# Kernel optimization log

Measured on AMD Instinct MI355X. Metric: run time of the kernel, lower is better.

Reference implementation:

```python
import jax, jax.numpy as jnp
import numpy as np

B = 512
NODES_PER_GRAPH = 256
N = B * NODES_PER_GRAPH
IN_DIM = 128
HID = 128
PAD_VALUE = -10000.0


def setup_inputs() -> dict:
    key = jax.random.key(0)
    ks = jax.random.split(key, 10)
    inp = {
        "last_node_batch": jax.random.normal(ks[0], (B, IN_DIM), jnp.float32),
        "h": jax.random.normal(ks[1], (N, HID), jnp.float32),
        # NodeEmbed: Linear(in_dim, hidden_dim)
        "W_embed": jax.random.normal(ks[2], (IN_DIM, HID), jnp.float32) / np.sqrt(IN_DIM),
        "b_embed": jnp.zeros((HID,), jnp.float32),
        # Linear_3(2H, 2H, 2)
        "W1": jax.random.normal(ks[3], (2 * HID, 2 * HID), jnp.float32) / np.sqrt(2 * HID),
        "b1": jnp.zeros((2 * HID,), jnp.float32),
        "W2": jax.random.normal(ks[4], (2 * HID, 2 * HID), jnp.float32) / np.sqrt(2 * HID),
        "b2": jnp.zeros((2 * HID,), jnp.float32),
        "W3": jax.random.normal(ks[5], (2 * HID, 2), jnp.float32) / np.sqrt(2 * HID),
        "b3": jnp.zeros((2,), jnp.float32),
        # ragged batch encoded as sorted segment ids (graph id per node)
        "segment_ids": jnp.repeat(jnp.arange(B, dtype=jnp.int64), NODES_PER_GRAPH),
        "max_nodes": NODES_PER_GRAPH,
    }
    return inp


def reference(last_node_batch, h, W_embed, b_embed, W1, b1, W2, b2, W3, b3,
              segment_ids, max_nodes):
    n = h.shape[0]
    b = last_node_batch.shape[0]
    # per-graph node embed, broadcast to each node of its graph (repeat+cat loop)
    node_embed = last_node_batch @ W_embed + b_embed          # [B, H]
    bcast = node_embed[segment_ids]                           # [N, H]
    stack = jnp.concatenate([h, bcast], axis=1)               # [N, 2H]
    # Linear_3 MLP
    out = jnp.tanh(stack @ W1 + b1)
    out = jnp.tanh(out @ W2 + b2)
    edges = out @ W3 + b3                                     # [N, 2]
    # unbatch + pad_sequence(padding_value=-10000), then flatten(1, -1)
    counts = jax.ops.segment_sum(jnp.ones((n,), jnp.int32), segment_ids, num_segments=b)
    offsets = jnp.cumsum(counts) - counts                     # start index of each graph
    pos = jnp.arange(n) - offsets[segment_ids]                # position within graph
    padded = jnp.full((b, max_nodes, 2), PAD_VALUE, dtype=edges.dtype)
    padded = padded.at[segment_ids, pos].set(edges)
    return padded.reshape(b, max_nodes * 2)
```

## Files before the change

kernel.cpp:

```cpp
#include <hip/hip_runtime.h>


typedef __attribute__((ext_vector_type(8))) short s16x8;
typedef __attribute__((ext_vector_type(4))) float f32x4;

#define MT   64
#define K2   256
#define HID  128
#define LDK  264

__device__ __forceinline__ float b2f(unsigned short u) {
  return __builtin_bit_cast(float, (unsigned int)u << 16);
}
__device__ __forceinline__ unsigned short f2b(float f) {
  unsigned int u = __builtin_bit_cast(unsigned int, f);
  u += 0x7fffu + ((u >> 16) & 1u);
  return (unsigned short)(u >> 16);
}
__device__ __forceinline__ float fast_tanh(float x) {
  float ax = __builtin_fabsf(x);
  float t  = __builtin_amdgcn_exp2f(ax * -2.885390081777927f);
  float r  = (1.0f - t) * __builtin_amdgcn_rcpf(1.0f + t);
  return __builtin_copysignf(r, x);
}

__global__ void probe_kernel(const unsigned int* __restrict__ wraw,
                             unsigned int* __restrict__ flag) {
  const int t = threadIdx.x;
  unsigned int w = wraw[t];
  unsigned int e = (w >> 7) & 0xFFu;
  unsigned long long m = __ballot(e >= 96 && e < 128);
  if (t == 0) flag[0] = (__popcll(m) >= 32) ? 1u : 0u;
}

__global__ __launch_bounds__(256) void prep_kernel(
    const void* __restrict__ last, const void* __restrict__ Wemb,
    const void* __restrict__ bemb,
    const void* __restrict__ W1, const void* __restrict__ W2,
    const void* __restrict__ b1, const void* __restrict__ b2,
    const void* __restrict__ W3, const void* __restrict__ b3,
    unsigned short* __restrict__ W1T, unsigned short* __restrict__ W2T,
    unsigned short* __restrict__ emb,
    float* __restrict__ bias1f, float* __restrict__ bias2f,
    float* __restrict__ w3fp, float* __restrict__ bias3f,
    const unsigned int* __restrict__ flag)
{
  const int blk = blockIdx.x, t = threadIdx.x;
  const bool is16 = flag[0] != 0u;
  if (blk < 128) {
    const void*     S = (blk < 64) ? W1 : W2;
    unsigned short* D = (blk < 64) ? W1T : W2T;
    const int b  = blk & 63;
    const int k0 = (b & 7) * 32, n0 = (b >> 3) * 32;
    #pragma unroll
    for (int q = 0; q < 4; ++q) {
      int idx = t + 256 * q;
      int ln = idx >> 5, lk = idx & 31;
      unsigned short v;
      if (is16) v = ((const unsigned short*)S)[(k0 + lk) * K2 + (n0 + ln)];
      else      v = f2b(((const float*)S)[(k0 + lk) * K2 + (n0 + ln)]);
      D[(n0 + ln) * K2 + (k0 + lk)] = v;
    }
  } else if (blk < 384) {
    __shared__ float lrow[2][HID];
    const int eb = blk - 128;
    const int half = t >> 7, j = t & 127;
    const int brow = eb * 2 + half;
    lrow[half][j] = is16 ? b2f(((const unsigned short*)last)[brow * HID + j])
                         : ((const float*)last)[brow * HID + j];
    __syncthreads();
    float acc = is16 ? b2f(((const unsigned short*)bemb)[j])
                     : ((const float*)bemb)[j];
    if (is16) {
      const unsigned short* w = (const unsigned short*)Wemb;
      #pragma unroll 4
      for (int k = 0; k < HID; ++k) acc += lrow[half][k] * b2f(w[k * HID + j]);
    } else {
      const float* w = (const float*)Wemb;
      #pragma unroll 4
      for (int k = 0; k < HID; ++k) acc += lrow[half][k] * w[k * HID + j];
    }
    emb[brow * HID + j] = f2b(acc);
  } else {
    if (is16) {
      bias1f[t] = b2f(((const unsigned short*)b1)[t]);
      bias2f[t] = b2f(((const unsigned short*)b2)[t]);
      w3fp[t]       = b2f(((const unsigned short*)W3)[t]);
      w3fp[t + 256] = b2f(((const unsigned short*)W3)[t + 256]);
      if (t < 2) bias3f[t] = b2f(((const unsigned short*)b3)[t]);
    } else {
      bias1f[t] = ((const float*)b1)[t];
      bias2f[t] = ((const float*)b2)[t];
      w3fp[t]       = ((const float*)W3)[t];
      w3fp[t + 256] = ((const float*)W3)[t + 256];
      if (t < 2) bias3f[t] = ((const float*)b3)[t];
    }
  }
}

template <int MODE>
__global__ __launch_bounds__(256, 2) void mlp_kernel(
    const void* __restrict__ h,
    const void* __restrict__ last, const void* __restrict__ Wemb,
    const void* __restrict__ bemb,
    const void* __restrict__ W1raw, const void* __restrict__ b1,
    const void* __restrict__ W2raw, const void* __restrict__ b2,
    const void* __restrict__ W3,   const void* __restrict__ b3,
    const unsigned short* __restrict__ W1T,
    const unsigned short* __restrict__ W2T,
    const unsigned short* __restrict__ embws,
    const float* __restrict__ bias1f, const float* __restrict__ bias2f,
    const float* __restrict__ w3fp,   const float* __restrict__ bias3f,
    void* __restrict__ out,
    const unsigned int* __restrict__ flag)
{
  __shared__ __align__(16) unsigned short smA[MT * LDK];
  __shared__ __align__(16) unsigned short embRow[HID];
  __shared__ float w3s[2 * K2];
  __shared__ float b3s[2];
  __shared__ unsigned int flagLds;

  const int t    = threadIdx.x;
  const int lane = t & 63, wave = t >> 6;
  const int quad = lane >> 4, l16 = lane & 15;
  const int base = blockIdx.x * MT;
  const int seg  = base >> 8;

  bool is16;
  if (MODE == 2) {
    if (t < 64) {
      unsigned int w = ((const unsigned int*)Wemb)[t];
      unsigned int e = (w >> 7) & 0xFFu;
      unsigned long long m = __ballot(e >= 96 && e < 128);
      if (t == 0) flagLds = (__popcll(m) >= 32) ? 1u : 0u;
    }
    __syncthreads();
    is16 = flagLds != 0u;
  } else {
    is16 = flag[0] != 0u;
  }

  if (is16) {
    const uint4* hp = (const uint4*)h;
    #pragma unroll
    for (int i = 0; i < 4; ++i) {
      int id = t + 256 * i;
      int r = id >> 4, c = id & 15;
      *(uint4*)&smA[r * LDK + c * 8] = hp[(size_t)(base + r) * 16 + c];
    }
  } else {
    const float4* hf = (const float4*)h;
    #pragma unroll
    for (int i = 0; i < 8; ++i) {
      int id = t + 256 * i;
      int r = id >> 5, c = id & 31;
      float4 v = hf[(size_t)(base + r) * 32 + c];
      ushort4 u;
      u.x = f2b(v.x); u.y = f2b(v.y); u.z = f2b(v.z); u.w = f2b(v.w);
      *(ushort4*)&smA[r * LDK + c * 4] = u;
    }
  }

  if (MODE == 0) {
    const uint4* ep = (const uint4*)(embws + seg * HID);
    #pragma unroll
    for (int i = 0; i < 4; ++i) {
      int id = t + 256 * i;
      int r = id >> 4, c = id & 15;
      *(uint4*)&smA[r * LDK + HID + c * 8] = ep[c];
    }
  } else {
    if (t < HID) {
      float acc;
      if (is16) {
        acc = b2f(((const unsigned short*)bemb)[t]);
        const unsigned short* lp = (const unsigned short*)last + seg * HID;
        const unsigned short* wp = (const unsigned short*)Wemb;
        #pragma unroll 4
        for (int k = 0; k < HID; ++k) acc += b2f(lp[k]) * b2f(wp[k * HID + t]);
      } else {
        acc = ((const float*)bemb)[t];
        const float* lp = (const float*)last + seg * HID;
        const float* wp = (const float*)Wemb;
        #pragma unroll 4
        for (int k = 0; k < HID; ++k) acc += lp[k] * wp[k * HID + t];
      }
      embRow[t] = f2b(acc);
    }
    __syncthreads();
    #pragma unroll
    for (int i = 0; i < 4; ++i) {
      int id = t + 256 * i;
      int r = id >> 4, c = id & 15;
      *(uint4*)&smA[r * LDK + HID + c * 8] = *(const uint4*)&embRow[c * 8];
    }
  }

  if (MODE == 0) {
    w3s[t] = w3fp[t]; w3s[t + 256] = w3fp[t + 256];
    if (t < 2) b3s[t] = bias3f[t];
  } else {
    if (is16) {
      w3s[t]       = b2f(((const unsigned short*)W3)[t]);
      w3s[t + 256] = b2f(((const unsigned short*)W3)[t + 256]);
      if (t < 2) b3s[t] = b2f(((const unsigned short*)b3)[t]);
    } else {
      w3s[t]       = ((const float*)W3)[t];
      w3s[t + 256] = ((const float*)W3)[t + 256];
      if (t < 2) b3s[t] = ((const float*)b3)[t];
    }
  }
  __syncthreads();

  auto run_layer = [&](const unsigned short* __restrict__ WT,
                       const void* __restrict__ Wraw,
                       const float* __restrict__ biasF,
                       const void* __restrict__ biasRaw) {
    f32x4 acc[4][4];
    #pragma unroll
    for (int i = 0; i < 4; ++i)
      #pragma unroll
      for (int c = 0; c < 4; ++c)
        acc[i][c] = f32x4{0.f, 0.f, 0.f, 0.f};

    #pragma unroll 2
    for (int kk = 0; kk < 8; ++kk) {
      s16x8 a[4], b[4];
      #pragma unroll
      for (int i = 0; i < 4; ++i)
        a[i] = *(const s16x8*)&smA[(i * 16 + l16) * LDK + kk * 32 + quad * 8];
      if (MODE < 2) {
        #pragma unroll
        for (int c = 0; c < 4; ++c)
          b[c] = *(const s16x8*)&WT[(size_t)(wave * 64 + c * 16 + l16) * K2
                                    + kk * 32 + quad * 8];
      } else {
        if (is16) {
          const unsigned short* wp = (const unsigned short*)Wraw;
          #pragma unroll
          for (int c = 0; c < 4; ++c) {
            s16x8 bb;
            #pragma unroll
            for (int j = 0; j < 8; ++j)
              bb[j] = (short)wp[(size_t)(kk * 32 + quad * 8 + j) * K2
                                + wave * 64 + c * 16 + l16];
            b[c] = bb;
          }
        } else {
          const float* wp = (const float*)Wraw;
          #pragma unroll
          for (int c = 0; c < 4; ++c) {
            s16x8 bb;
            #pragma unroll
            for (int j = 0; j < 8; ++j)
              bb[j] = (short)f2b(wp[(size_t)(kk * 32 + quad * 8 + j) * K2
                                    + wave * 64 + c * 16 + l16]);
            b[c] = bb;
          }
        }
      }
      #pragma unroll
      for (int i = 0; i < 4; ++i)
        #pragma unroll
        for (int c = 0; c < 4; ++c)
          acc[i][c] = __builtin_amdgcn_mfma_f32_16x16x32_bf16(
              a[i], b[c], acc[i][c], 0, 0, 0);
    }
    float bl[4];
    #pragma unroll
    for (int c = 0; c < 4; ++c) {
      int n = wave * 64 + c * 16 + l16;
      if (MODE == 0) bl[c] = biasF[n];
      else bl[c] = is16 ? b2f(((const unsigned short*)biasRaw)[n])
                        : ((const float*)biasRaw)[n];
    }
    __syncthreads();
    #pragma unroll
    for (int i = 0; i < 4; ++i)
      #pragma unroll
      for (int c = 0; c < 4; ++c)
        #pragma unroll
        for (int rg = 0; rg < 4; ++rg)
          smA[(i * 16 + quad * 4 + rg) * LDK + wave * 64 + c * 16 + l16] =
              f2b(fast_tanh(acc[i][c][rg] + bl[c]));
    __syncthreads();
  };

  run_layer(W1T, W1raw, bias1f, b1);
  run_layer(W2T, W2raw, bias2f, b2);

  if (t < 128) {
    const int r = t >> 1, e = t & 1;
    float s = b3s[e];
    #pragma unroll 8
    for (int c = 0; c < 32; ++c) {
      s16x8 v = *(const s16x8*)&smA[r * LDK + c * 8];
      #pragma unroll
      for (int i = 0; i < 8; ++i)
        s += b2f((unsigned short)v[i]) * w3s[(c * 8 + i) * 2 + e];
    }
    size_t idx = (size_t)(base + r) * 2 + e;
    if (is16) ((unsigned short*)out)[idx] = f2b(s);
    else      ((float*)out)[idx] = s;
  }
}

extern "C" void kernel_launch(void* const* d_in, const int* in_sizes, int n_in,
                              void* d_out, int out_size, void* d_ws, size_t ws_size,
                              hipStream_t stream) {
  (void)in_sizes; (void)n_in; (void)out_size;
  const void* last = d_in[0];
  const void* h    = d_in[1];
  const void* Wemb = d_in[2];
  const void* bemb = d_in[3];
  const void* W1   = d_in[4];
  const void* b1   = d_in[5];
  const void* W2   = d_in[6];
  const void* b2   = d_in[7];
  const void* W3   = d_in[8];
  const void* b3   = d_in[9];

  char* ws = (char*)d_ws;

  if (ws_size >= 397324) {
    unsigned short* W1T  = (unsigned short*)(ws);
    unsigned short* W2T  = (unsigned short*)(ws + 131072);
    unsigned short* emb  = (unsigned short*)(ws + 262144);
    float* bias1f        = (float*)(ws + 393216);
    float* bias2f        = (float*)(ws + 394240);
    float* w3fp          = (float*)(ws + 395264);
    float* bias3f        = (float*)(ws + 397312);
    unsigned int* flag   = (unsigned int*)(ws + 397320);
    probe_kernel<<<dim3(1), dim3(64), 0, stream>>>((const unsigned int*)Wemb, flag);
    prep_kernel<<<dim3(385), dim3(256), 0, stream>>>(
        last, Wemb, bemb, W1, W2, b1, b2, W3, b3,
        W1T, W2T, emb, bias1f, bias2f, w3fp, bias3f, flag);
    mlp_kernel<0><<<dim3(2048), dim3(256), 0, stream>>>(
        h, last, Wemb, bemb, W1, b1, W2, b2, W3, b3,
        W1T, W2T, emb, bias1f, bias2f, w3fp, bias3f, d_out, flag);
  } else if (ws_size >= 262208) {
    unsigned short* W1T  = (unsigned short*)(ws);
    unsigned short* W2T  = (unsigned short*)(ws + 131072);
    unsigned int* flag   = (unsigned int*)(ws + 262144);
    probe_kernel<<<dim3(1), dim3(64), 0, stream>>>((const unsigned int*)Wemb, flag);
    prep_kernel<<<dim3(128), dim3(256), 0, stream>>>(
        last, Wemb, bemb, W1, W2, b1, b2, W3, b3,
        W1T, W2T, W1T, (float*)ws, (float*)ws, (float*)ws, (float*)ws, flag);
    mlp_kernel<1><<<dim3(2048), dim3(256), 0, stream>>>(
        h, last, Wemb, bemb, W1, b1, W2, b2, W3, b3,
        W1T, W2T, nullptr, nullptr, nullptr, nullptr, nullptr, d_out, flag);
  } else {
    mlp_kernel<2><<<dim3(2048), dim3(256), 0, stream>>>(
        h, last, Wemb, bemb, W1, b1, W2, b2, W3, b3,
        nullptr, nullptr, nullptr, nullptr, nullptr, nullptr, nullptr,
        d_out, nullptr);
  }
}
```

Baseline: 193.9 us.

## Fold graph embedding into per-graph layer-1 bias and fuse into single MLP kernel

The embed half of layer 1 is no longer a GEMM over every node. Each block computes emb @ W1[128:] plus b1 as a per-graph bias, which halves the K of the first MFMA GEMM. The probe and prep kernels are merged into a single packing kernel that writes weights in an MFMA-fragment layout. The main kernel now handles 128-row tiles with 512 threads and splits the output head across four threads per row. Each block recomputes the small per-graph embedding and bias GEMVs, which adds scalar work and a larger LDS footprint per block.

Result: faster. 184.5 us (-4.9%).

```diff
diff --git a/kernel.cpp b/kernel.cpp
--- a/kernel.cpp
+++ b/kernel.cpp
@@ -4,9 +4,8 @@
 typedef __attribute__((ext_vector_type(8))) short s16x8;
 typedef __attribute__((ext_vector_type(4))) float f32x4;
 
-#define MT   64
 #define K2   256
-#define HID  128
+#define KH   128
 #define LDK  264
 
 __device__ __forceinline__ float b2f(unsigned short u) {
@@ -23,128 +22,77 @@
   float r  = (1.0f - t) * __builtin_amdgcn_rcpf(1.0f + t);
   return __builtin_copysignf(r, x);
 }
-
-__global__ void probe_kernel(const unsigned int* __restrict__ wraw,
-                             unsigned int* __restrict__ flag) {
-  const int t = threadIdx.x;
+__device__ __forceinline__ unsigned int probe_is16(const unsigned int* wraw,
+                                                   int t) {
   unsigned int w = wraw[t];
   unsigned int e = (w >> 7) & 0xFFu;
   unsigned long long m = __ballot(e >= 96 && e < 128);
-  if (t == 0) flag[0] = (__popcll(m) >= 32) ? 1u : 0u;
-}
-
-__global__ __launch_bounds__(256) void prep_kernel(
-    const void* __restrict__ last, const void* __restrict__ Wemb,
-    const void* __restrict__ bemb,
+  return (__popcll(m) >= 32) ? 1u : 0u;
+}
+
+__global__ __launch_bounds__(256) void prep_pack(
     const void* __restrict__ W1, const void* __restrict__ W2,
-    const void* __restrict__ b1, const void* __restrict__ b2,
-    const void* __restrict__ W3, const void* __restrict__ b3,
-    unsigned short* __restrict__ W1T, unsigned short* __restrict__ W2T,
-    unsigned short* __restrict__ emb,
-    float* __restrict__ bias1f, float* __restrict__ bias2f,
-    float* __restrict__ w3fp, float* __restrict__ bias3f,
-    const unsigned int* __restrict__ flag)
+    const void* __restrict__ Wemb,
+    unsigned short* __restrict__ W1P, unsigned short* __restrict__ W2P)
 {
+  __shared__ unsigned int flagLds;
   const int blk = blockIdx.x, t = threadIdx.x;
-  const bool is16 = flag[0] != 0u;
-  if (blk < 128) {
-    const void*     S = (blk < 64) ? W1 : W2;
-    unsigned short* D = (blk < 64) ? W1T : W2T;
-    const int b  = blk & 63;
-    const int k0 = (b & 7) * 32, n0 = (b >> 3) * 32;
-    #pragma unroll
-    for (int q = 0; q < 4; ++q) {
-      int idx = t + 256 * q;
-      int ln = idx >> 5, lk = idx & 31;
-      unsigned short v;
-      if (is16) v = ((const unsigned short*)S)[(k0 + lk) * K2 + (n0 + ln)];
-      else      v = f2b(((const float*)S)[(k0 + lk) * K2 + (n0 + ln)]);
-      D[(n0 + ln) * K2 + (k0 + lk)] = v;
-    }
-  } else if (blk < 384) {
-    __shared__ float lrow[2][HID];
-    const int eb = blk - 128;
-    const int half = t >> 7, j = t & 127;
-    const int brow = eb * 2 + half;
-    lrow[half][j] = is16 ? b2f(((const unsigned short*)last)[brow * HID + j])
-                         : ((const float*)last)[brow * HID + j];
-    __syncthreads();
-    float acc = is16 ? b2f(((const unsigned short*)bemb)[j])
-                     : ((const float*)bemb)[j];
-    if (is16) {
-      const unsigned short* w = (const unsigned short*)Wemb;
-      #pragma unroll 4
-      for (int k = 0; k < HID; ++k) acc += lrow[half][k] * b2f(w[k * HID + j]);
-    } else {
-      const float* w = (const float*)Wemb;
-      #pragma unroll 4
-      for (int k = 0; k < HID; ++k) acc += lrow[half][k] * w[k * HID + j];
-    }
-    emb[brow * HID + j] = f2b(acc);
-  } else {
-    if (is16) {
-      bias1f[t] = b2f(((const unsigned short*)b1)[t]);
-      bias2f[t] = b2f(((const unsigned short*)b2)[t]);
-      w3fp[t]       = b2f(((const unsigned short*)W3)[t]);
-      w3fp[t + 256] = b2f(((const unsigned short*)W3)[t + 256]);
-      if (t < 2) bias3f[t] = b2f(((const unsigned short*)b3)[t]);
-    } else {
-      bias1f[t] = ((const float*)b1)[t];
-      bias2f[t] = ((const float*)b2)[t];
-      w3fp[t]       = ((const float*)W3)[t];
-      w3fp[t + 256] = ((const float*)W3)[t + 256];
-      if (t < 2) bias3f[t] = ((const float*)b3)[t];
-    }
-  }
-}
-
-template <int MODE>
-__global__ __launch_bounds__(256, 2) void mlp_kernel(
-    const void* __restrict__ h,
-    const void* __restrict__ last, const void* __restrict__ Wemb,
-    const void* __restrict__ bemb,
-    const void* __restrict__ W1raw, const void* __restrict__ b1,
-    const void* __restrict__ W2raw, const void* __restrict__ b2,
-    const void* __restrict__ W3,   const void* __restrict__ b3,
-    const unsigned short* __restrict__ W1T,
-    const unsigned short* __restrict__ W2T,
-    const unsigned short* __restrict__ embws,
-    const float* __restrict__ bias1f, const float* __restrict__ bias2f,
-    const float* __restrict__ w3fp,   const float* __restrict__ bias3f,
-    void* __restrict__ out,
-    const unsigned int* __restrict__ flag)
+  if (t < 64) { unsigned int f = probe_is16((const unsigned int*)Wemb, t);
+                if (t == 0) flagLds = f; }
+  __syncthreads();
+  const bool is16 = flagLds != 0u;
+
+  const void* S; unsigned short* D; int k0, n0, pk;
+  if (blk < 32) { S = W1; D = W1P; pk = 2048;
+                  k0 = (blk & 3) * 32; n0 = (blk >> 2) * 32; }
+  else { int b = blk - 32; S = W2; D = W2P; pk = 4096;
+         k0 = (b & 7) * 32; n0 = (b >> 3) * 32; }
+  #pragma unroll
+  for (int q = 0; q < 4; ++q) {
+    int idx = t + 256 * q;
+    int ln = idx & 31, lk = idx >> 5;
+    int n = n0 + ln, k = k0 + lk;
+    unsigned short v = is16 ? ((const unsigned short*)S)[k * K2 + n]
+                            : f2b(((const float*)S)[k * K2 + n]);
+    D[(n >> 4) * pk + (k >> 3) * 128 + (n & 15) * 8 + (k & 7)] = v;
+  }
+}
+
+__global__ __launch_bounds__(512, 4) void mlp_fused(
+    const void* __restrict__ h,     const void* __restrict__ last,
+    const void* __restrict__ Wemb,  const void* __restrict__ bemb,
+    const void* __restrict__ W1,    const void* __restrict__ b1,
+    const void* __restrict__ b2,    const void* __restrict__ W3,
+    const void* __restrict__ b3,
+    const unsigned short* __restrict__ W1P,
+    const unsigned short* __restrict__ W2P,
+    void* __restrict__ out)
 {
-  __shared__ __align__(16) unsigned short smA[MT * LDK];
-  __shared__ __align__(16) unsigned short embRow[HID];
+  __shared__ __align__(16) unsigned short smA[128 * LDK];
+  __shared__ float embf[KH];
+  __shared__ float ebias[K2];
   __shared__ float w3s[2 * K2];
   __shared__ float b3s[2];
+  __shared__ float headp[128 * 8];
   __shared__ unsigned int flagLds;
 
   const int t    = threadIdx.x;
-  const int lane = t & 63, wave = t >> 6;
+  const int lane = t & 63, w = t >> 6;
+  const int wr = w >> 2, wc = w & 3;
   const int quad = lane >> 4, l16 = lane & 15;
-  const int base = blockIdx.x * MT;
-  const int seg  = base >> 8;
-
-  bool is16;
-  if (MODE == 2) {
-    if (t < 64) {
-      unsigned int w = ((const unsigned int*)Wemb)[t];
-      unsigned int e = (w >> 7) & 0xFFu;
-      unsigned long long m = __ballot(e >= 96 && e < 128);
-      if (t == 0) flagLds = (__popcll(m) >= 32) ? 1u : 0u;
-    }
-    __syncthreads();
-    is16 = flagLds != 0u;
-  } else {
-    is16 = flag[0] != 0u;
-  }
+  const int base = blockIdx.x * 128;
+  const int g    = base >> 8;
+
+  if (t < 64) { unsigned int f = probe_is16((const unsigned int*)Wemb, t);
+                if (t == 0) flagLds = f; }
+  __syncthreads();
+  const bool is16 = flagLds != 0u;
 
   if (is16) {
     const uint4* hp = (const uint4*)h;
     #pragma unroll
     for (int i = 0; i < 4; ++i) {
-      int id = t + 256 * i;
+      int id = t + 512 * i;
       int r = id >> 4, c = id & 15;
       *(uint4*)&smA[r * LDK + c * 8] = hp[(size_t)(base + r) * 16 + c];
     }
@@ -152,7 +100,7 @@
     const float4* hf = (const float4*)h;
     #pragma unroll
     for (int i = 0; i < 8; ++i) {
-      int id = t + 256 * i;
+      int id = t + 512 * i;
       int r = id >> 5, c = id & 31;
       float4 v = hf[(size_t)(base + r) * 32 + c];
       ushort4 u;
@@ -160,145 +108,142 @@
       *(ushort4*)&smA[r * LDK + c * 4] = u;
     }
   }
-
-  if (MODE == 0) {
-    const uint4* ep = (const uint4*)(embws + seg * HID);
-    #pragma unroll
-    for (int i = 0; i < 4; ++i) {
-      int id = t + 256 * i;
-      int r = id >> 4, c = id & 15;
-      *(uint4*)&smA[r * LDK + HID + c * 8] = ep[c];
-    }
-  } else {
-    if (t < HID) {
-      float acc;
-      if (is16) {
-        acc = b2f(((const unsigned short*)bemb)[t]);
-        const unsigned short* lp = (const unsigned short*)last + seg * HID;
-        const unsigned short* wp = (const unsigned short*)Wemb;
-        #pragma unroll 4
-        for (int k = 0; k < HID; ++k) acc += b2f(lp[k]) * b2f(wp[k * HID + t]);
-      } else {
-        acc = ((const float*)bemb)[t];
-        const float* lp = (const float*)last + seg * HID;
-        const float* wp = (const float*)Wemb;
-        #pragma unroll 4
-        for (int k = 0; k < HID; ++k) acc += lp[k] * wp[k * HID + t];
+  w3s[t] = is16 ? b2f(((const unsigned short*)W3)[t]) : ((const float*)W3)[t];
+  if (t < 2)
+    b3s[t] = is16 ? b2f(((const unsigned short*)b3)[t]) : ((const float*)b3)[t];
+  if (t < KH) {
+    float acc;
+    if (is16) {
+      acc = b2f(((const unsigned short*)bemb)[t]);
+      const unsigned short* lp = (const unsigned short*)last + g * KH;
+      const unsigned short* wp = (const unsigned short*)Wemb;
+      #pragma unroll 4
+      for (int k = 0; k < KH; ++k) acc += b2f(lp[k]) * b2f(wp[k * KH + t]);
+    } else {
+      acc = ((const float*)bemb)[t];
+      const float* lp = (const float*)last + g * KH;
+      const float* wp = (const float*)Wemb;
+      #pragma unroll 4
+      for (int k = 0; k < KH; ++k) acc += lp[k] * wp[k * KH + t];
+    }
+    embf[t] = acc;
+  }
+  __syncthreads();
+
+  if (t < K2) {
+    float e = is16 ? b2f(((const unsigned short*)b1)[t]) : ((const float*)b1)[t];
+    if (is16) {
+      const unsigned short* wp = (const unsigned short*)W1 + (size_t)KH * K2;
+      #pragma unroll 4
+      for (int k = 0; k < KH; ++k) e += embf[k] * b2f(wp[k * K2 + t]);
+    } else {
+      const float* wp = (const float*)W1 + (size_t)KH * K2;
+      #pragma unroll 4
+      for (int k = 0; k < KH; ++k) e += embf[k] * wp[k * K2 + t];
+    }
+    ebias[t] = e;
+  }
+
+  f32x4 acc[4][4];
+  #pragma unroll
+  for (int i = 0; i < 4; ++i)
+    #pragma unroll
+    for (int c = 0; c < 4; ++c) acc[i][c] = f32x4{0.f, 0.f, 0.f, 0.f};
+  #pragma unroll
+  for (int kk = 0; kk < 4; ++kk) {
+    s16x8 a[4], b[4];
+    #pragma unroll
+    for (int i = 0; i < 4; ++i)
+      a[i] = *(const s16x8*)&smA[(wr * 64 + i * 16 + l16) * LDK
+                                 + kk * 32 + quad * 8];
+    #pragma unroll
+    for (int c = 0; c < 4; ++c)
+      b[c] = *(const s16x8*)&W1P[(wc * 4 + c) * 2048
+                                 + (kk * 4 + quad) * 128 + l16 * 8];
+    #pragma unroll
+    for (int i = 0; i < 4; ++i)
+      #pragma unroll
+      for (int c = 0; c < 4; ++c)
+        acc[i][c] = __builtin_amdgcn_mfma_f32_16x16x32_bf16(
+            a[i], b[c], acc[i][c], 0, 0, 0);
+  }
+  __syncthreads();
+  #pragma unroll
+  for (int i = 0; i < 4; ++i)
+    #pragma unroll
+    for (int c = 0; c < 4; ++c) {
+      int col = wc * 64 + c * 16 + l16;
+      #pragma unroll
+      for (int rg = 0; rg < 4; ++rg)
+        smA[(wr * 64 + i * 16 + quad * 4 + rg) * LDK + col] =
+            f2b(fast_tanh(acc[i][c][rg] + ebias[col]));
+    }
+  __syncthreads();
+
+  #pragma unroll
+  for (int i = 0; i < 4; ++i)
+    #pragma unroll
+    for (int c = 0; c < 4; ++c) acc[i][c] = f32x4{0.f, 0.f, 0.f, 0.f};
+  #pragma unroll 2
+  for (int kk = 0; kk < 8; ++kk) {
+    s16x8 a[4], b[4];
+    #pragma unroll
+    for (int i = 0; i < 4; ++i)
+      a[i] = *(const s16x8*)&smA[(wr * 64 + i * 16 + l16) * LDK
+                                 + kk * 32 + quad * 8];
+    #pragma unroll
+    for (int c = 0; c < 4; ++c)
+      b[c] = *(const s16x8*)&W2P[(wc * 4 + c) * 4096
+                                 + (kk * 4 + quad) * 128 + l16 * 8];
+    #pragma unroll
+    for (int i = 0; i < 4; ++i)
+      #pragma unroll
+      for (int c = 0; c < 4; ++c)
+        acc[i][c] = __builtin_amdgcn_mfma_f32_16x16x32_bf16(
+            a[i], b[c], acc[i][c], 0, 0, 0);
+  }
+  float bl[4];
+  #pragma unroll
+  for (int c = 0; c < 4; ++c) {
+    int n = wc * 64 + c * 16 + l16;
+    bl[c] = is16 ? b2f(((const unsigned short*)b2)[n]) : ((const float*)b2)[n];
+  }
+  __syncthreads();
+  #pragma unroll
+  for (int i = 0; i < 4; ++i)
+    #pragma unroll
+    for (int c = 0; c < 4; ++c) {
+      int col = wc * 64 + c * 16 + l16;
+      #pragma unroll
+      for (int rg = 0; rg < 4; ++rg)
+        smA[(wr * 64 + i * 16 + quad * 4 + rg) * LDK + col] =
+            f2b(fast_tanh(acc[i][c][rg] + bl[c]));
+    }
+  __syncthreads();
+
+  {
+    const int r = t >> 2, q = t & 3;
+    float s0 = 0.f, s1 = 0.f;
+    #pragma unroll
+    for (int cc = 0; cc < 8; ++cc) {
+      int c8 = q * 8 + ((cc + r) & 7);
+      s16x8 v = *(const s16x8*)&smA[r * LDK + c8 * 8];
+      #pragma unroll
+      for (int j = 0; j < 8; ++j) {
+        float f = b2f((unsigned short)v[j]);
+        int k = c8 * 8 + j;
+        s0 += f * w3s[2 * k];
+        s1 += f * w3s[2 * k + 1];
       }
-      embRow[t] = f2b(acc);
-    }
-    __syncthreads();
-    #pragma unroll
-    for (int i = 0; i < 4; ++i) {
-      int id = t + 256 * i;
-      int r = id >> 4, c = id & 15;
-      *(uint4*)&smA[r * LDK + HID + c * 8] = *(const uint4*)&embRow[c * 8];
-    }
-  }
-
-  if (MODE == 0) {
-    w3s[t] = w3fp[t]; w3s[t + 256] = w3fp[t + 256];
-    if (t < 2) b3s[t] = bias3f[t];
-  } else {
-    if (is16) {
-      w3s[t]       = b2f(((const unsigned short*)W3)[t]);
-      w3s[t + 256] = b2f(((const unsigned short*)W3)[t + 256]);
-      if (t < 2) b3s[t] = b2f(((const unsigned short*)b3)[t]);
-    } else {
-      w3s[t]       = ((const float*)W3)[t];
-      w3s[t + 256] = ((const float*)W3)[t + 256];
-      if (t < 2) b3s[t] = ((const float*)b3)[t];
-    }
-  }
-  __syncthreads();
-
-  auto run_layer = [&](const unsigned short* __restrict__ WT,
-                       const void* __restrict__ Wraw,
-                       const float* __restrict__ biasF,
-                       const void* __restrict__ biasRaw) {
-    f32x4 acc[4][4];
-    #pragma unroll
-    for (int i = 0; i < 4; ++i)
-      #pragma unroll
-      for (int c = 0; c < 4; ++c)
-        acc[i][c] = f32x4{0.f, 0.f, 0.f, 0.f};
-
-    #pragma unroll 2
-    for (int kk = 0; kk < 8; ++kk) {
-      s16x8 a[4], b[4];
-      #pragma unroll
-      for (int i = 0; i < 4; ++i)
-        a[i] = *(const s16x8*)&smA[(i * 16 + l16) * LDK + kk * 32 + quad * 8];
-      if (MODE < 2) {
-        #pragma unroll
-        for (int c = 0; c < 4; ++c)
-          b[c] = *(const s16x8*)&WT[(size_t)(wave * 64 + c * 16 + l16) * K2
-                                    + kk * 32 + quad * 8];
-      } else {
-        if (is16) {
-          const unsigned short* wp = (const unsigned short*)Wraw;
-          #pragma unroll
-          for (int c = 0; c < 4; ++c) {
-            s16x8 bb;
-            #pragma unroll
-            for (int j = 0; j < 8; ++j)
-              bb[j] = (short)wp[(size_t)(kk * 32 + quad * 8 + j) * K2
-                                + wave * 64 + c * 16 + l16];
-            b[c] = bb;
-          }
-        } else {
-          const float* wp = (const float*)Wraw;
-          #pragma unroll
-          for (int c = 0; c < 4; ++c) {
-            s16x8 bb;
-            #pragma unroll
-            for (int j = 0; j < 8; ++j)
-              bb[j] = (short)f2b(wp[(size_t)(kk * 32 + quad * 8 + j) * K2
-                                    + wave * 64 + c * 16 + l16]);
-            b[c] = bb;
-          }
-        }
-      }
-      #pragma unroll
-      for (int i = 0; i < 4; ++i)
-        #pragma unroll
-        for (int c = 0; c < 4; ++c)
-          acc[i][c] = __builtin_amdgcn_mfma_f32_16x16x32_bf16(
-              a[i], b[c], acc[i][c], 0, 0, 0);
-    }
-    float bl[4];
-    #pragma unroll
-    for (int c = 0; c < 4; ++c) {
-      int n = wave * 64 + c * 16 + l16;
-      if (MODE == 0) bl[c] = biasF[n];
-      else bl[c] = is16 ? b2f(((const unsigned short*)biasRaw)[n])
-                        : ((const float*)biasRaw)[n];
-    }
-    __syncthreads();
-    #pragma unroll
-    for (int i = 0; i < 4; ++i)
-      #pragma unroll
-      for (int c = 0; c < 4; ++c)
-        #pragma unroll
-        for (int rg = 0; rg < 4; ++rg)
-          smA[(i * 16 + quad * 4 + rg) * LDK + wave * 64 + c * 16 + l16] =
-              f2b(fast_tanh(acc[i][c][rg] + bl[c]));
-    __syncthreads();
-  };
-
-  run_layer(W1T, W1raw, bias1f, b1);
-  run_layer(W2T, W2raw, bias2f, b2);
-
-  if (t < 128) {
+    }
+    headp[r * 8 + q * 2 + 0] = s0;
+    headp[r * 8 + q * 2 + 1] = s1;
+  }
+  __syncthreads();
+  if (t < 256) {
     const int r = t >> 1, e = t & 1;
-    float s = b3s[e];
-    #pragma unroll 8
-    for (int c = 0; c < 32; ++c) {
-      s16x8 v = *(const s16x8*)&smA[r * LDK + c * 8];
-      #pragma unroll
-      for (int i = 0; i < 8; ++i)
-        s += b2f((unsigned short)v[i]) * w3s[(c * 8 + i) * 2 + e];
-    }
+    float s = b3s[e] + headp[r * 8 + e] + headp[r * 8 + 2 + e]
+            + headp[r * 8 + 4 + e] + headp[r * 8 + 6 + e];
     size_t idx = (size_t)(base + r) * 2 + e;
     if (is16) ((unsigned short*)out)[idx] = f2b(s);
     else      ((float*)out)[idx] = s;
@@ -308,7 +253,7 @@
 extern "C" void kernel_launch(void* const* d_in, const int* in_sizes, int n_in,
                               void* d_out, int out_size, void* d_ws, size_t ws_size,
                               hipStream_t stream) {
-  (void)in_sizes; (void)n_in; (void)out_size;
+  (void)in_sizes; (void)n_in; (void)out_size; (void)ws_size;
   const void* last = d_in[0];
   const void* h    = d_in[1];
   const void* Wemb = d_in[2];
@@ -321,38 +266,10 @@
   const void* b3   = d_in[9];
 
   char* ws = (char*)d_ws;
-
-  if (ws_size >= 397324) {
-    unsigned short* W1T  = (unsigned short*)(ws);
-    unsigned short* W2T  = (unsigned short*)(ws + 131072);
-    unsigned short* emb  = (unsigned short*)(ws + 262144);
-    float* bias1f        = (float*)(ws + 393216);
-    float* bias2f        = (float*)(ws + 394240);
-    float* w3fp          = (float*)(ws + 395264);
-    float* bias3f        = (float*)(ws + 397312);
-    unsigned int* flag   = (unsigned int*)(ws + 397320);
-    probe_kernel<<<dim3(1), dim3(64), 0, stream>>>((const unsigned int*)Wemb, flag);
-    prep_kernel<<<dim3(385), dim3(256), 0, stream>>>(
-        last, Wemb, bemb, W1, W2, b1, b2, W3, b3,
-        W1T, W2T, emb, bias1f, bias2f, w3fp, bias3f, flag);
-    mlp_kernel<0><<<dim3(2048), dim3(256), 0, stream>>>(
-        h, last, Wemb, bemb, W1, b1, W2, b2, W3, b3,
-        W1T, W2T, emb, bias1f, bias2f, w3fp, bias3f, d_out, flag);
-  } else if (ws_size >= 262208) {
-    unsigned short* W1T  = (unsigned short*)(ws);
-    unsigned short* W2T  = (unsigned short*)(ws + 131072);
-    unsigned int* flag   = (unsigned int*)(ws + 262144);
-    probe_kernel<<<dim3(1), dim3(64), 0, stream>>>((const unsigned int*)Wemb, flag);
-    prep_kernel<<<dim3(128), dim3(256), 0, stream>>>(
-        last, Wemb, bemb, W1, W2, b1, b2, W3, b3,
-        W1T, W2T, W1T, (float*)ws, (float*)ws, (float*)ws, (float*)ws, flag);
-    mlp_kernel<1><<<dim3(2048), dim3(256), 0, stream>>>(
-        h, last, Wemb, bemb, W1, b1, W2, b2, W3, b3,
-        W1T, W2T, nullptr, nullptr, nullptr, nullptr, nullptr, d_out, flag);
-  } else {
-    mlp_kernel<2><<<dim3(2048), dim3(256), 0, stream>>>(
-        h, last, Wemb, bemb, W1, b1, W2, b2, W3, b3,
-        nullptr, nullptr, nullptr, nullptr, nullptr, nullptr, nullptr,
-        d_out, nullptr);
-  }
-}
+  unsigned short* W1P = (unsigned short*)(ws);
+  unsigned short* W2P = (unsigned short*)(ws + 65536);
+
+  prep_pack<<<dim3(96), dim3(256), 0, stream>>>(W1, W2, Wemb, W1P, W2P);
+  mlp_fused<<<dim3(1024), dim3(512), 0, stream>>>(
+      h, last, Wemb, bemb, W1, b1, b2, W3, b3, W1P, W2P, d_out);
+}
```
